# Optimization experiments

Hardware: AMD Instinct MI355X
Metric: run time of the kernel (lower is better)

Reference implementation:

```python
import jax, jax.numpy as jnp
import numpy as np

N = 100000      # nodes
E = 1600000     # edges (before self-loops)
IN = 128        # in_dim
HID = 128       # hidden_dim
H = 4           # heads
D = HID // H    # head_dim = 32
L = 3           # n_layers
G = 128         # graphs in batch
NEG_SLOPE = 0.2 # PyG GATConv default leaky_relu slope
BN_EPS = 1e-5


def setup_inputs() -> dict:
    key = jax.random.key(0)
    ks = jax.random.split(key, 16)
    x = jax.random.normal(ks[0], (N, IN), dtype=jnp.float32)
    edge_index = jax.random.randint(ks[1], (2, E), 0, N, dtype=jnp.int64)
    batch = jnp.sort(jax.random.randint(ks[2], (N,), 0, G, dtype=jnp.int64))
    # stacked per-layer GATConv params (in_dim == hidden_dim so all layers stack)
    W = jax.random.normal(ks[3], (L, HID, HID), dtype=jnp.float32) * (1.0 / np.sqrt(HID))
    att_src = jax.random.normal(ks[4], (L, H, D), dtype=jnp.float32) * 0.1
    att_dst = jax.random.normal(ks[5], (L, H, D), dtype=jnp.float32) * 0.1
    bias = jax.random.normal(ks[6], (L, HID), dtype=jnp.float32) * 0.01
    # BatchNorm1d (eval mode: running stats)
    gamma = 1.0 + 0.1 * jax.random.normal(ks[7], (L, HID), dtype=jnp.float32)
    beta = 0.01 * jax.random.normal(ks[8], (L, HID), dtype=jnp.float32)
    bn_mean = jnp.zeros((L, HID), dtype=jnp.float32)
    bn_var = jnp.ones((L, HID), dtype=jnp.float32)
    # MLP head: Linear(HID, HID//2) -> ReLU -> Linear(HID//2, 1)
    Wh1 = jax.random.normal(ks[9], (HID, HID // 2), dtype=jnp.float32) * (1.0 / np.sqrt(HID))
    bh1 = jnp.zeros((HID // 2,), dtype=jnp.float32)
    Wh2 = jax.random.normal(ks[10], (HID // 2, 1), dtype=jnp.float32) * (1.0 / np.sqrt(HID // 2))
    bh2 = jnp.zeros((1,), dtype=jnp.float32)
    return {"x": x, "edge_index": edge_index, "batch": batch, "W": W,
            "att_src": att_src, "att_dst": att_dst, "bias": bias,
            "gamma": gamma, "beta": beta, "bn_mean": bn_mean, "bn_var": bn_var,
            "Wh1": Wh1, "bh1": bh1, "Wh2": Wh2, "bh2": bh2}


def _gat_conv(x, src, dst, W_l, asrc, adst, b):
    # x: [N, F_in]; src/dst: [E+N] (self-loops included); returns [N, H*D]
    h = (x @ W_l).reshape(N, H, D)                      # [N,H,D]
    a_s = jnp.einsum('nhd,hd->nh', h, asrc)             # [N,H]
    a_d = jnp.einsum('nhd,hd->nh', h, adst)
    e = jax.nn.leaky_relu(a_s[src] + a_d[dst], NEG_SLOPE)  # [Etot,H]
    # segment softmax over incoming edges per destination node
    e_max = jax.ops.segment_max(e, dst, num_segments=N)    # [N,H]
    p = jnp.exp(e - e_max[dst])
    denom = jax.ops.segment_sum(p, dst, num_segments=N)    # [N,H]
    alpha = p / (denom[dst] + 1e-16)                        # [Etot,H]
    msg = h[src] * alpha[:, :, None]                        # [Etot,H,D]
    out = jax.ops.segment_sum(msg, dst, num_segments=N)     # [N,H,D]
    return out.reshape(N, H * D) + b


def reference(x, edge_index, batch, W, att_src, att_dst, bias,
              gamma, beta, bn_mean, bn_var, Wh1, bh1, Wh2, bh2):
    # add self-loops once (PyG GATConv default add_self_loops=True)
    loop = jnp.arange(N, dtype=edge_index.dtype)
    src = jnp.concatenate([edge_index[0], loop])
    dst = jnp.concatenate([edge_index[1], loop])
    for l in range(L):
        x = _gat_conv(x, src, dst, W[l], att_src[l], att_dst[l], bias[l])
        x = jnp.maximum(x, 0.0)
        # BatchNorm1d, eval mode (dropout is identity in eval)
        x = (x - bn_mean[l]) * (gamma[l] / jnp.sqrt(bn_var[l] + BN_EPS)) + beta[l]
    # global mean pool over graphs
    sums = jax.ops.segment_sum(x, batch, num_segments=G)            # [G,HID]
    cnts = jax.ops.segment_sum(jnp.ones((N,), x.dtype), batch, num_segments=G)
    pooled = sums / jnp.maximum(cnts, 1.0)[:, None]
    hdn = jnp.maximum(pooled @ Wh1 + bh1, 0.0)
    return (hdn @ Wh2 + bh2).squeeze(-1)                            # [G]
```

## Files before the change

kernel.cpp:

```cpp
#include <hip/hip_runtime.h>
#include <hip/hip_fp16.h>


typedef __bf16 bf16x8 __attribute__((ext_vector_type(8)));
typedef float  f32x4  __attribute__((ext_vector_type(4)));
typedef unsigned int u32x4 __attribute__((ext_vector_type(4)));

#define WLSZ 36864

#define MAXBKT 800
#define BCAP   4096

__global__ __launch_bounds__(256)
void k_bucket(const int* __restrict__ ei, unsigned int* __restrict__ bkt,
              int* __restrict__ bcnt, float* __restrict__ gsum,
              int* __restrict__ gcnt, int Ne, int Nn, int nbkt, int Gg) {
    __shared__ int lcnt[MAXBKT];
    __shared__ int lbase[MAXBKT];
    int tid = threadIdx.x;
    int gid = blockIdx.x * 256 + tid;
    if (gid < Gg * 128) gsum[gid] = 0.f;
    if (gid < Gg) gcnt[gid] = 0;
    for (int i = tid; i < nbkt; i += 256) lcnt[i] = 0;
    __syncthreads();
    int chunk0 = blockIdx.x * 2048;
    int nnz = Ne + Nn;
    for (int i = 0; i < 8; ++i) {
        int e = chunk0 + i * 256 + tid;
        if (e < nnz) {
            int d = (e < Ne) ? ei[Ne + e] : (e - Ne);
            atomicAdd(&lcnt[d >> 7], 1);
        }
    }
    __syncthreads();
    for (int b = tid; b < nbkt; b += 256) {
        int c = lcnt[b];
        lbase[b] = (c > 0) ? atomicAdd(&bcnt[b], c) : 0;
        lcnt[b] = 0;
    }
    __syncthreads();
    for (int i = 0; i < 8; ++i) {
        int e = chunk0 + i * 256 + tid;
        if (e < nnz) {
            int s, d;
            if (e < Ne) { s = ei[e]; d = ei[Ne + e]; }
            else        { s = e - Ne; d = e - Ne; }
            int b = d >> 7;
            int r = atomicAdd(&lcnt[b], 1);
            bkt[(long)b * BCAP + lbase[b] + r] = ((unsigned)s << 7) | (unsigned)(d & 127);
        }
    }
}

__global__ __launch_bounds__(1024)
void k_bktscan(const int* __restrict__ bcnt, int* __restrict__ bktbase, int nbkt) {
    __shared__ int s0[1024], s1[1024];
    int t = threadIdx.x;
    int v = (t < nbkt) ? bcnt[t] : 0;
    s0[t] = v;
    __syncthreads();
    int* src = s0; int* dst = s1;
    for (int off = 1; off < 1024; off <<= 1) {
        int x = src[t];
        if (t >= off) x += src[t - off];
        dst[t] = x;
        __syncthreads();
        int* tw = src; src = dst; dst = tw;
    }
    if (t < nbkt) bktbase[t] = src[t] - v;
}

__global__ __launch_bounds__(256)
void k_bscatter2(const unsigned int* __restrict__ bkt, const int* __restrict__ bcnt,
                 const int* __restrict__ bktbase, int* __restrict__ rowptr,
                 int* __restrict__ colv, int Nn, int nnz) {
    __shared__ int h[128], sc0[128], sc1[128];
    int b = blockIdx.x;
    int tid = threadIdx.x;
    if (tid < 128) h[tid] = 0;
    __syncthreads();
    int cnt = bcnt[b];
    int base = bktbase[b];
    const unsigned int* bp = bkt + (long)b * BCAP;
    for (int i = tid; i < cnt; i += 256) atomicAdd(&h[bp[i] & 127], 1);
    __syncthreads();
    if (tid < 128) sc0[tid] = h[tid];
    __syncthreads();
    int* src = sc0; int* dst = sc1;
    for (int off = 1; off < 128; off <<= 1) {
        if (tid < 128) {
            int x = src[tid];
            if (tid >= off) x += src[tid - off];
            dst[tid] = x;
        }
        __syncthreads();
        int* tw = src; src = dst; dst = tw;
    }
    int node = b * 128 + tid;
    if (tid < 128) {
        int excl = src[tid] - h[tid];
        int st = base + excl;
        h[tid] = st;
        if (node < Nn) rowptr[node] = st;
    }
    if (b == 0 && tid == 0) rowptr[Nn] = nnz;
    __syncthreads();
    for (int i = tid; i < cnt; i += 256) {
        unsigned int e = bp[i];
        int pos = atomicAdd(&h[e & 127], 1);
        colv[pos] = (int)(e >> 7);
    }
}

__device__ __forceinline__ int foff(int l, int d, int n, int k) {
    int ct = n >> 4, li = n & 15;
    int ks = k >> 5, bq = (k >> 3) & 3, j = k & 7;
    return l * WLSZ + (((ks * 18) + d * 9 + ct) * 64 + (bq << 4) + li) * 8 + j;
}

__global__ void k_prep(const float* __restrict__ gamma, const float* __restrict__ beta,
                       const float* __restrict__ mean, const float* __restrict__ var,
                       float* __restrict__ bn_mul, float* __restrict__ bn_add,
                       const float* __restrict__ W, const float* __restrict__ asrc,
                       const float* __restrict__ adst, __bf16* __restrict__ WF) {
    int gid = blockIdx.x * 256 + threadIdx.x;
    if (gid < 384) {
        float sc = gamma[gid] / sqrtf(var[gid] + 1e-5f);
        bn_mul[gid] = sc;
        bn_add[gid] = beta[gid] - mean[gid] * sc;
    }
    if (gid < 3 * 128 * 128) {
        int l = gid >> 14;
        int k = (gid >> 7) & 127;
        int n = gid & 127;
        float f = W[gid];
        __bf16 h = (__bf16)f;
        WF[foff(l, 0, n, k)] = h;
        WF[foff(l, 1, n, k)] = (__bf16)(f - (float)h);
    }
    if (gid < 3 * 128 * 8) {
        int l = gid >> 10;
        int r = gid & 1023;
        int k = r >> 3;
        int j = r & 7;
        int hh = j & 3;
        const float* av = (j < 4 ? asrc : adst) + l * 128 + hh * 32;
        const float* wp = W + l * 16384 + k * 128 + hh * 32;
        float sum = 0.f;
#pragma unroll
        for (int d = 0; d < 32; ++d) sum = fmaf(wp[d], av[d], sum);
        __bf16 h = (__bf16)sum;
        WF[foff(l, 0, 128 + j, k)] = h;
        WF[foff(l, 1, 128 + j, k)] = (__bf16)(sum - (float)h);
    }
    if (gid < 3 * 128 * 8) {
        int l = gid >> 10;
        int r = gid & 1023;
        int k = r >> 3;
        int j = r & 7;
        WF[foff(l, 0, 136 + j, k)] = (__bf16)0.f;
        WF[foff(l, 1, 136 + j, k)] = (__bf16)0.f;
    }
}

__global__ __launch_bounds__(256)
void k_gemm_mfma(const float* __restrict__ X, const __bf16* __restrict__ WF,
                 __half* __restrict__ Hout,
                 float* __restrict__ as_, float* __restrict__ ad_, int Nn) {
    int t = threadIdx.x;
    int w = t >> 6;
    int lane = t & 63;
    int li = lane & 15;
    int b  = lane >> 4;
    long rowBase = (long)blockIdx.x * 128 + w * 32;

    f32x4 acc[2][9];
#pragma unroll
    for (int rt = 0; rt < 2; ++rt)
#pragma unroll
        for (int ct = 0; ct < 9; ++ct) acc[rt][ct] = (f32x4){0.f, 0.f, 0.f, 0.f};

    long rA[2];
#pragma unroll
    for (int rt = 0; rt < 2; ++rt) {
        long r = rowBase + rt * 16 + li;
        rA[rt] = (r > Nn - 1) ? (Nn - 1) : r;
    }

#pragma unroll
    for (int ks = 0; ks < 4; ++ks) {
        int k0 = ks * 32 + 8 * b;
        bf16x8 ahi[2], alo[2];
#pragma unroll
        for (int rt = 0; rt < 2; ++rt) {
            const float* xp = X + rA[rt] * 128 + k0;
            float4 f0 = *(const float4*)xp;
            float4 f1 = *(const float4*)(xp + 4);
            float af[8] = {f0.x, f0.y, f0.z, f0.w, f1.x, f1.y, f1.z, f1.w};
#pragma unroll
            for (int j = 0; j < 8; ++j) {
                __bf16 h = (__bf16)af[j];
                ahi[rt][j] = h;
                alo[rt][j] = (__bf16)(af[j] - (float)h);
            }
        }
        const __bf16* wk = WF + (ks * 18) * 512 + lane * 8;
#pragma unroll
        for (int ct = 0; ct < 9; ++ct) {
            bf16x8 bhi = *(const bf16x8*)(wk + ct * 512);
            bf16x8 blo = *(const bf16x8*)(wk + (9 + ct) * 512);
#pragma unroll
            for (int rt = 0; rt < 2; ++rt) {
                acc[rt][ct] = __builtin_amdgcn_mfma_f32_16x16x32_bf16(bhi, ahi[rt], acc[rt][ct], 0, 0, 0);
                acc[rt][ct] = __builtin_amdgcn_mfma_f32_16x16x32_bf16(bhi, alo[rt], acc[rt][ct], 0, 0, 0);
                acc[rt][ct] = __builtin_amdgcn_mfma_f32_16x16x32_bf16(blo, ahi[rt], acc[rt][ct], 0, 0, 0);
            }
        }
    }

#pragma unroll
    for (int rt = 0; rt < 2; ++rt) {
        long r = rowBase + rt * 16 + li;
        if (r < Nn) {
            __half* op = Hout + r * 128 + 4 * b;
#pragma unroll
            for (int ct = 0; ct < 8; ++ct) {
                union { __half2 h2[2]; uint2 u; } pk;
                pk.h2[0] = __floats2half2_rn(acc[rt][ct][0], acc[rt][ct][1]);
                pk.h2[1] = __floats2half2_rn(acc[rt][ct][2], acc[rt][ct][3]);
                *(uint2*)(op + ct * 16) = pk.u;
            }
            if (b == 0)
                *(float4*)(as_ + 4 * r) = make_float4(acc[rt][8][0], acc[rt][8][1],
                                                      acc[rt][8][2], acc[rt][8][3]);
            else if (b == 1)
                *(float4*)(ad_ + 4 * r) = make_float4(acc[rt][8][0], acc[rt][8][1],
                                                      acc[rt][8][2], acc[rt][8][3]);
        }
    }
}

#define LEAKY(x) ((x) > 0.f ? (x) : 0.2f * (x))

__global__ __launch_bounds__(256)
void k_aggregate(const __half* __restrict__ Hb, const float* __restrict__ as_,
                 const float* __restrict__ ad_, const int* __restrict__ rowptr,
                 const int* __restrict__ col, const float* __restrict__ bias,
                 const float* __restrict__ bn_mul, const float* __restrict__ bn_add,
                 float* __restrict__ Xout, int Nn) {
    __shared__ int2 s_pk[4][64][4];
    int w = threadIdx.x >> 6;
    int n = (blockIdx.x << 2) + w;
    if (n >= Nn) return;
    int lane = threadIdx.x & 63;
    int start = rowptr[n], end = rowptr[n + 1];
    int deg = end - start;

    if (deg <= 64) {
        int hh = lane & 3;
        int slot = lane >> 2;
        float adn = ad_[4 * n + hh];
        float esc[4]; int scl[4];
#pragma unroll
        for (int c = 0; c < 4; ++c) {
            int eidx = (c << 4) + slot;
            float e = -1e30f; int s = 0;
            if (eidx < deg) {
                s = col[start + eidx];
                e = LEAKY(as_[4 * s + hh] + adn);
            }
            esc[c] = e; scl[c] = s;
        }
        float m = fmaxf(fmaxf(esc[0], esc[1]), fmaxf(esc[2], esc[3]));
#pragma unroll
        for (int msk = 4; msk < 64; msk <<= 1) m = fmaxf(m, __shfl_xor(m, msk, 64));
        float p[4];
        float den = 0.f;
#pragma unroll
        for (int c = 0; c < 4; ++c) { p[c] = __expf(esc[c] - m); den += p[c]; }
#pragma unroll
        for (int msk = 4; msk < 64; msk <<= 1) den += __shfl_xor(den, msk, 64);
        float inv = 1.f / (den + 1e-16f);
#pragma unroll
        for (int c = 0; c < 4; ++c) {
            int2 pk;
            pk.x = scl[c] << 8;
            pk.y = __float_as_int(p[c] * inv);
            s_pk[w][(c << 4) + slot][hh] = pk;
        }

        int quarter = lane >> 4;
        int li = lane & 15;
        int hB = li >> 2;
        int cByte = li << 4;
        const char* hb8 = (const char*)Hb;
        float acc[8];
#pragma unroll
        for (int i = 0; i < 8; ++i) acc[i] = 0.f;

        int nit = (deg + 7) >> 3;
        int2 pk0 = s_pk[w][quarter][hB];
        int2 pk1 = s_pk[w][quarter + 4][hB];
        float a0 = __int_as_float(pk0.y);
        float a1 = __int_as_float(pk1.y);
        u32x4 r0 = *(const u32x4*)(hb8 + pk0.x + cByte);
        u32x4 r1 = *(const u32x4*)(hb8 + pk1.x + cByte);
        for (int it = 1; it < nit; ++it) {
            int e0 = (it << 3) + quarter;
            int2 q0 = s_pk[w][e0][hB];
            int2 q1 = s_pk[w][e0 + 4][hB];
            u32x4 t0 = *(const u32x4*)(hb8 + q0.x + cByte);
            u32x4 t1 = *(const u32x4*)(hb8 + q1.x + cByte);
            const __half* h0 = (const __half*)&r0;
            const __half* h1 = (const __half*)&r1;
#pragma unroll
            for (int q = 0; q < 8; ++q) {
                acc[q] = fmaf(__half2float(h0[q]), a0, acc[q]);
                acc[q] = fmaf(__half2float(h1[q]), a1, acc[q]);
            }
            r0 = t0; r1 = t1;
            a0 = __int_as_float(q0.y);
            a1 = __int_as_float(q1.y);
        }
        {
            const __half* h0 = (const __half*)&r0;
            const __half* h1 = (const __half*)&r1;
#pragma unroll
            for (int q = 0; q < 8; ++q) {
                acc[q] = fmaf(__half2float(h0[q]), a0, acc[q]);
                acc[q] = fmaf(__half2float(h1[q]), a1, acc[q]);
            }
        }
#pragma unroll
        for (int i = 0; i < 8; ++i) {
            float v = acc[i];
            v += __shfl_xor(v, 16, 64);
            v += __shfl_xor(v, 32, 64);
            acc[i] = v;
        }
        if (lane < 16) {
            int c0 = li << 3;
            float4 bz0 = *(const float4*)(bias + c0);
            float4 bz1 = *(const float4*)(bias + c0 + 4);
            float4 m0 = *(const float4*)(bn_mul + c0);
            float4 m1 = *(const float4*)(bn_mul + c0 + 4);
            float4 a0v = *(const float4*)(bn_add + c0);
            float4 a1v = *(const float4*)(bn_add + c0 + 4);
            float4 o0, o1;
            o0.x = fmaf(fmaxf(acc[0] + bz0.x, 0.f), m0.x, a0v.x);
            o0.y = fmaf(fmaxf(acc[1] + bz0.y, 0.f), m0.y, a0v.y);
            o0.z = fmaf(fmaxf(acc[2] + bz0.z, 0.f), m0.z, a0v.z);
            o0.w = fmaf(fmaxf(acc[3] + bz0.w, 0.f), m0.w, a0v.w);
            o1.x = fmaf(fmaxf(acc[4] + bz1.x, 0.f), m1.x, a1v.x);
            o1.y = fmaf(fmaxf(acc[5] + bz1.y, 0.f), m1.y, a1v.y);
            o1.z = fmaf(fmaxf(acc[6] + bz1.z, 0.f), m1.z, a1v.z);
            o1.w = fmaf(fmaxf(acc[7] + bz1.w, 0.f), m1.w, a1v.w);
            *(float4*)(Xout + (long)n * 128 + c0)     = o0;
            *(float4*)(Xout + (long)n * 128 + c0 + 4) = o1;
        }
        return;
    }

    int hh = lane & 3;
    float adn = ad_[n * 4 + hh];
    float m = -1e30f;
    for (int base = start; base < end; base += 16) {
        int idx = base + (lane >> 2);
        float sc = -1e30f;
        if (idx < end) {
            int s = col[idx];
            float e = as_[s * 4 + hh] + adn;
            sc = LEAKY(e);
        }
        m = fmaxf(m, sc);
    }
    for (int msk = 4; msk < 64; msk <<= 1) m = fmaxf(m, __shfl_xor(m, msk, 64));
    float den = 0.f;
    for (int base = start; base < end; base += 16) {
        int idx = base + (lane >> 2);
        if (idx < end) {
            int s = col[idx];
            float e = as_[s * 4 + hh] + adn;
            e = LEAKY(e);
            den += __expf(e - m);
        }
    }
    for (int msk = 4; msk < 64; msk <<= 1) den += __shfl_xor(den, msk, 64);
    int hB = lane >> 4;
    float mB   = __shfl(m, hB, 64);
    float invB = 1.f / (__shfl(den, hB, 64) + 1e-16f);
    float adB  = ad_[n * 4 + hB];
    int c0 = lane << 1;
    float acc0 = 0.f, acc1 = 0.f;
    for (int i = start; i < end; ++i) {
        int s = col[i];
        float e = as_[s * 4 + hB] + adB;
        e = LEAKY(e);
        float alpha = __expf(e - mB) * invB;
        float2 hv = __half22float2(*(const __half2*)(Hb + (long)s * 128 + c0));
        acc0 = fmaf(hv.x, alpha, acc0);
        acc1 = fmaf(hv.y, alpha, acc1);
    }
    float v0 = acc0 + bias[c0], v1 = acc1 + bias[c0 + 1];
    v0 = fmaxf(v0, 0.f); v1 = fmaxf(v1, 0.f);
    v0 = fmaf(v0, bn_mul[c0], bn_add[c0]);
    v1 = fmaf(v1, bn_mul[c0 + 1], bn_add[c0 + 1]);
    *(float2*)(Xout + (long)n * 128 + c0) = make_float2(v0, v1);
}

__global__ __launch_bounds__(128)
void k_pool(const float* __restrict__ X, const int* __restrict__ batch,
            float* __restrict__ gsum, int* __restrict__ gcnt, int Nn) {
    int c = threadIdx.x;
    int n0 = blockIdx.x * 64;
    if (n0 >= Nn) return;
    int nend = (n0 + 64 < Nn) ? n0 + 64 : Nn;
    float local = 0.f;
    int gcur = batch[n0];
    int cnt = 0;
    for (int n = n0; n < nend; ++n) {
        int g = batch[n];
        if (g != gcur) {
            atomicAdd(&gsum[gcur * 128 + c], local);
            if (c == 0) atomicAdd(&gcnt[gcur], cnt);
            local = 0.f; cnt = 0; gcur = g;
        }
        local += X[(long)n * 128 + c];
        cnt += 1;
    }
    atomicAdd(&gsum[gcur * 128 + c], local);
    if (c == 0) atomicAdd(&gcnt[gcur], cnt);
}

__global__ __launch_bounds__(64)
void k_head(const float* __restrict__ gsum, const int* __restrict__ gcnt,
            const float* __restrict__ Wh1, const float* __restrict__ bh1,
            const float* __restrict__ Wh2, const float* __restrict__ bh2,
            float* __restrict__ outp) {
    __shared__ float pooled[128];
    int g = blockIdx.x;
    int j = threadIdx.x;
    int cnt = gcnt[g];
    float inv = 1.f / (float)(cnt > 1 ? cnt : 1);
    pooled[j]      = gsum[g * 128 + j] * inv;
    pooled[j + 64] = gsum[g * 128 + 64 + j] * inv;
    __syncthreads();
    float acc = bh1[j];
    for (int k = 0; k < 128; ++k) acc = fmaf(pooled[k], Wh1[k * 64 + j], acc);
    acc = fmaxf(acc, 0.f);
    float prod = acc * Wh2[j];
    for (int msk = 1; msk < 64; msk <<= 1) prod += __shfl_xor(prod, msk, 64);
    if (j == 0) outp[g] = prod + bh2[0];
}

extern "C" void kernel_launch(void* const* d_in, const int* in_sizes, int n_in,
                              void* d_out, int out_size, void* d_ws, size_t ws_size,
                              hipStream_t stream) {
    const float* x       = (const float*)d_in[0];
    const int*   ei      = (const int*)d_in[1];
    const int*   batch   = (const int*)d_in[2];
    const float* W       = (const float*)d_in[3];
    const float* att_src = (const float*)d_in[4];
    const float* att_dst = (const float*)d_in[5];
    const float* bias    = (const float*)d_in[6];
    const float* gamma   = (const float*)d_in[7];
    const float* beta    = (const float*)d_in[8];
    const float* bn_mean = (const float*)d_in[9];
    const float* bn_var  = (const float*)d_in[10];
    const float* Wh1     = (const float*)d_in[11];
    const float* bh1     = (const float*)d_in[12];
    const float* Wh2     = (const float*)d_in[13];
    const float* bh2     = (const float*)d_in[14];
    float* out = (float*)d_out;

    const int Nn = in_sizes[0] / 128;
    const int Ne = in_sizes[1] / 2;
    const int Gg = out_size;
    const int nnz = Ne + Nn;
    const int nbkt = (Nn + 127) / 128;

    char* ws = (char*)d_ws;
    size_t off = 0;
    auto alloc = [&](size_t bytes) -> char* {
        char* p = ws + off;
        off = (off + bytes + 255) & ~(size_t)255;
        return p;
    };
    float*        bufA    = (float*)alloc((size_t)Nn * 128 * 4);
    __half*       bufH    = (__half*)alloc((size_t)Nn * 128 * 2);
    float*        as_     = (float*)alloc((size_t)Nn * 4 * 4);
    float*        ad_     = (float*)alloc((size_t)Nn * 4 * 4);
    int*          rowptr  = (int*)alloc((size_t)(Nn + 1) * 4);
    int*          col     = (int*)alloc((size_t)nnz * 4);
    float*        bn_mul  = (float*)alloc(384 * 4);
    float*        bn_add  = (float*)alloc(384 * 4);
    float*        gsum    = (float*)alloc((size_t)Gg * 128 * 4);
    int*          gcnt    = (int*)alloc((size_t)Gg * 4);
    __bf16*       WtF     = (__bf16*)alloc((size_t)3 * WLSZ * 2);
    unsigned int* bkt     = (unsigned int*)alloc((size_t)nbkt * BCAP * 4);
    int*          bcnt    = (int*)alloc((size_t)nbkt * 4);
    int*          bktbase = (int*)alloc((size_t)nbkt * 4);

    hipMemsetAsync(bcnt, 0, (size_t)nbkt * 4, stream);
    k_prep<<<192, 256, 0, stream>>>(gamma, beta, bn_mean, bn_var, bn_mul, bn_add,
                                    W, att_src, att_dst, WtF);
    k_bucket<<<(nnz + 2047) / 2048, 256, 0, stream>>>(ei, bkt, bcnt, gsum, gcnt,
                                                      Ne, Nn, nbkt, Gg);
    k_bktscan<<<1, 1024, 0, stream>>>(bcnt, bktbase, nbkt);
    k_bscatter2<<<nbkt, 256, 0, stream>>>(bkt, bcnt, bktbase, rowptr, col, Nn, nnz);

    const float* cur = x;
    for (int l = 0; l < 3; ++l) {
        k_gemm_mfma<<<(Nn + 127) / 128, 256, 0, stream>>>(cur, WtF + l * WLSZ,
                                                          bufH, as_, ad_, Nn);
        k_aggregate<<<(Nn + 3) / 4, 256, 0, stream>>>(bufH, as_, ad_, rowptr, col,
                                                      bias + l * 128, bn_mul + l * 128,
                                                      bn_add + l * 128, bufA, Nn);
        cur = bufA;
    }

    k_pool<<<(Nn + 63) / 64, 128, 0, stream>>>(bufA, batch, gsum, gcnt, Nn);
    k_head<<<Gg, 64, 0, stream>>>(gsum, gcnt, Wh1, bh1, Wh2, bh2, out);
}
```

Measured before the change: 538.8 us.

## Replace bucketed CSR build with global per-node histogram, scan, and atomic scatter

Replaces the two-level bucket sort (shared-memory bucket counts, bucket buffer, per-bucket local sort) used to build the destination CSR with a direct approach. It runs a global per-node atomic histogram, a two-level scan into rowptr and cursor, and a second pass that atomically claims a slot per edge and writes the source index. This drops the intermediate bucket buffer and its read-back, but it reads edge_index twice and relies on global atomics with scattered writes to col. The within-row edge order now depends on atomic ordering, so summation order in the aggregation can vary between runs.

Result: slower. 715.8 us (+32.8%).

```diff
diff --git a/kernel.cpp b/kernel.cpp
--- a/kernel.cpp
+++ b/kernel.cpp
@@ -7,56 +7,38 @@
 typedef unsigned int u32x4 __attribute__((ext_vector_type(4)));
 
 #define WLSZ 36864
-
 #define MAXBKT 800
-#define BCAP   4096
 
 __global__ __launch_bounds__(256)
-void k_bucket(const int* __restrict__ ei, unsigned int* __restrict__ bkt,
-              int* __restrict__ bcnt, float* __restrict__ gsum,
-              int* __restrict__ gcnt, int Ne, int Nn, int nbkt, int Gg) {
-    __shared__ int lcnt[MAXBKT];
-    __shared__ int lbase[MAXBKT];
+void k_hist(const int* __restrict__ ei, int* __restrict__ rowcnt,
+            float* __restrict__ gsum, int* __restrict__ gcnt,
+            int Ne, int Nn, int Gg) {
     int tid = threadIdx.x;
     int gid = blockIdx.x * 256 + tid;
     if (gid < Gg * 128) gsum[gid] = 0.f;
     if (gid < Gg) gcnt[gid] = 0;
-    for (int i = tid; i < nbkt; i += 256) lcnt[i] = 0;
-    __syncthreads();
     int chunk0 = blockIdx.x * 2048;
     int nnz = Ne + Nn;
     for (int i = 0; i < 8; ++i) {
         int e = chunk0 + i * 256 + tid;
         if (e < nnz) {
             int d = (e < Ne) ? ei[Ne + e] : (e - Ne);
-            atomicAdd(&lcnt[d >> 7], 1);
-        }
-    }
-    __syncthreads();
-    for (int b = tid; b < nbkt; b += 256) {
-        int c = lcnt[b];
-        lbase[b] = (c > 0) ? atomicAdd(&bcnt[b], c) : 0;
-        lcnt[b] = 0;
-    }
-    __syncthreads();
-    for (int i = 0; i < 8; ++i) {
-        int e = chunk0 + i * 256 + tid;
-        if (e < nnz) {
-            int s, d;
-            if (e < Ne) { s = ei[e]; d = ei[Ne + e]; }
-            else        { s = e - Ne; d = e - Ne; }
-            int b = d >> 7;
-            int r = atomicAdd(&lcnt[b], 1);
-            bkt[(long)b * BCAP + lbase[b] + r] = ((unsigned)s << 7) | (unsigned)(d & 127);
+            atomicAdd(&rowcnt[d], 1);
         }
     }
 }
 
 __global__ __launch_bounds__(1024)
-void k_bktscan(const int* __restrict__ bcnt, int* __restrict__ bktbase, int nbkt) {
+void k_scan1(const int* __restrict__ rowcnt, int* __restrict__ chunkbase,
+             int nbkt, int Nn) {
     __shared__ int s0[1024], s1[1024];
     int t = threadIdx.x;
-    int v = (t < nbkt) ? bcnt[t] : 0;
+    int v = 0;
+    if (t < nbkt) {
+        int base = t * 128;
+        int lim = Nn - base; if (lim > 128) lim = 128;
+        for (int i = 0; i < lim; ++i) v += rowcnt[base + i];
+    }
     s0[t] = v;
     __syncthreads();
     int* src = s0; int* dst = s1;
@@ -67,48 +49,50 @@
         __syncthreads();
         int* tw = src; src = dst; dst = tw;
     }
-    if (t < nbkt) bktbase[t] = src[t] - v;
-}
-
-__global__ __launch_bounds__(256)
-void k_bscatter2(const unsigned int* __restrict__ bkt, const int* __restrict__ bcnt,
-                 const int* __restrict__ bktbase, int* __restrict__ rowptr,
-                 int* __restrict__ colv, int Nn, int nnz) {
-    __shared__ int h[128], sc0[128], sc1[128];
+    if (t < nbkt) chunkbase[t] = src[t] - v;
+}
+
+__global__ __launch_bounds__(128)
+void k_scan2(const int* __restrict__ rowcnt, const int* __restrict__ chunkbase,
+             int* __restrict__ rowptr, int* __restrict__ cursor, int Nn, int nnz) {
+    __shared__ int s0[128], s1[128];
     int b = blockIdx.x;
-    int tid = threadIdx.x;
-    if (tid < 128) h[tid] = 0;
+    int t = threadIdx.x;
+    int node = b * 128 + t;
+    int v = (node < Nn) ? rowcnt[node] : 0;
+    s0[t] = v;
     __syncthreads();
-    int cnt = bcnt[b];
-    int base = bktbase[b];
-    const unsigned int* bp = bkt + (long)b * BCAP;
-    for (int i = tid; i < cnt; i += 256) atomicAdd(&h[bp[i] & 127], 1);
-    __syncthreads();
-    if (tid < 128) sc0[tid] = h[tid];
-    __syncthreads();
-    int* src = sc0; int* dst = sc1;
+    int* src = s0; int* dst = s1;
     for (int off = 1; off < 128; off <<= 1) {
-        if (tid < 128) {
-            int x = src[tid];
-            if (tid >= off) x += src[tid - off];
-            dst[tid] = x;
-        }
+        int x = src[t];
+        if (t >= off) x += src[t - off];
+        dst[t] = x;
         __syncthreads();
         int* tw = src; src = dst; dst = tw;
     }
-    int node = b * 128 + tid;
-    if (tid < 128) {
-        int excl = src[tid] - h[tid];
-        int st = base + excl;
-        h[tid] = st;
-        if (node < Nn) rowptr[node] = st;
-    }
-    if (b == 0 && tid == 0) rowptr[Nn] = nnz;
-    __syncthreads();
-    for (int i = tid; i < cnt; i += 256) {
-        unsigned int e = bp[i];
-        int pos = atomicAdd(&h[e & 127], 1);
-        colv[pos] = (int)(e >> 7);
+    if (node < Nn) {
+        int st = chunkbase[b] + src[t] - v;
+        rowptr[node] = st;
+        cursor[node] = st;
+    }
+    if (b == 0 && t == 0) rowptr[Nn] = nnz;
+}
+
+__global__ __launch_bounds__(256)
+void k_scatter(const int* __restrict__ ei, int* __restrict__ cursor,
+               int* __restrict__ colv, int Ne, int Nn) {
+    int tid = threadIdx.x;
+    int chunk0 = blockIdx.x * 2048;
+    int nnz = Ne + Nn;
+    for (int i = 0; i < 8; ++i) {
+        int e = chunk0 + i * 256 + tid;
+        if (e < nnz) {
+            int s, d;
+            if (e < Ne) { s = ei[e]; d = ei[Ne + e]; }
+            else        { s = e - Ne; d = e - Ne; }
+            int pos = atomicAdd(&cursor[d], 1);
+            colv[pos] = s;
+        }
     }
 }
 
@@ -486,28 +470,29 @@
         off = (off + bytes + 255) & ~(size_t)255;
         return p;
     };
-    float*        bufA    = (float*)alloc((size_t)Nn * 128 * 4);
-    __half*       bufH    = (__half*)alloc((size_t)Nn * 128 * 2);
-    float*        as_     = (float*)alloc((size_t)Nn * 4 * 4);
-    float*        ad_     = (float*)alloc((size_t)Nn * 4 * 4);
-    int*          rowptr  = (int*)alloc((size_t)(Nn + 1) * 4);
-    int*          col     = (int*)alloc((size_t)nnz * 4);
-    float*        bn_mul  = (float*)alloc(384 * 4);
-    float*        bn_add  = (float*)alloc(384 * 4);
-    float*        gsum    = (float*)alloc((size_t)Gg * 128 * 4);
-    int*          gcnt    = (int*)alloc((size_t)Gg * 4);
-    __bf16*       WtF     = (__bf16*)alloc((size_t)3 * WLSZ * 2);
-    unsigned int* bkt     = (unsigned int*)alloc((size_t)nbkt * BCAP * 4);
-    int*          bcnt    = (int*)alloc((size_t)nbkt * 4);
-    int*          bktbase = (int*)alloc((size_t)nbkt * 4);
-
-    hipMemsetAsync(bcnt, 0, (size_t)nbkt * 4, stream);
+    float*        bufA      = (float*)alloc((size_t)Nn * 128 * 4);
+    __half*       bufH      = (__half*)alloc((size_t)Nn * 128 * 2);
+    float*        as_       = (float*)alloc((size_t)Nn * 4 * 4);
+    float*        ad_       = (float*)alloc((size_t)Nn * 4 * 4);
+    int*          rowptr    = (int*)alloc((size_t)(Nn + 1) * 4);
+    int*          col       = (int*)alloc((size_t)nnz * 4);
+    float*        bn_mul    = (float*)alloc(384 * 4);
+    float*        bn_add    = (float*)alloc(384 * 4);
+    float*        gsum      = (float*)alloc((size_t)Gg * 128 * 4);
+    int*          gcnt      = (int*)alloc((size_t)Gg * 4);
+    __bf16*       WtF       = (__bf16*)alloc((size_t)3 * WLSZ * 2);
+    int*          rowcnt    = (int*)alloc((size_t)Nn * 4);
+    int*          cursor    = (int*)alloc((size_t)Nn * 4);
+    int*          chunkbase = (int*)alloc((size_t)MAXBKT * 4);
+
+    hipMemsetAsync(rowcnt, 0, (size_t)Nn * 4, stream);
     k_prep<<<192, 256, 0, stream>>>(gamma, beta, bn_mean, bn_var, bn_mul, bn_add,
                                     W, att_src, att_dst, WtF);
-    k_bucket<<<(nnz + 2047) / 2048, 256, 0, stream>>>(ei, bkt, bcnt, gsum, gcnt,
-                                                      Ne, Nn, nbkt, Gg);
-    k_bktscan<<<1, 1024, 0, stream>>>(bcnt, bktbase, nbkt);
-    k_bscatter2<<<nbkt, 256, 0, stream>>>(bkt, bcnt, bktbase, rowptr, col, Nn, nnz);
+    k_hist<<<(nnz + 2047) / 2048, 256, 0, stream>>>(ei, rowcnt, gsum, gcnt,
+                                                    Ne, Nn, Gg);
+    k_scan1<<<1, 1024, 0, stream>>>(rowcnt, chunkbase, nbkt, Nn);
+    k_scan2<<<nbkt, 128, 0, stream>>>(rowcnt, chunkbase, rowptr, cursor, Nn, nnz);
+    k_scatter<<<(nnz + 2047) / 2048, 256, 0, stream>>>(ei, cursor, col, Ne, Nn);
 
     const float* cur = x;
     for (int l = 0; l < 3; ++l) {
```
